# Optimization experiments

Hardware: AMD Instinct MI355X
Metric: run time of the kernel (lower is better)

## Reference

```python
import jax, jax.numpy as jnp
import numpy as np

T, H, I, E, K = 4096, 2048, 768, 64, 8  # tokens, hidden, moe_intermediate, experts, top_k


def setup_inputs() -> dict:
    key = jax.random.key(0)
    k1, k2, k3, k4 = jax.random.split(key, 4)
    return {
        "x": jax.random.normal(k1, (T, H), jnp.float32),
        "gate_w": jax.random.normal(k2, (E, H), jnp.float32) * 0.02,          # router weight [E, H]
        "w_gate_up": jax.random.normal(k3, (E, H, 2 * I), jnp.float32) * 0.02,  # stacked gate|up [E, H, 2I]
        "w_down": jax.random.normal(k4, (E, I, H), jnp.float32) * 0.02,        # stacked down [E, I, H]
        "top_k": K,
    }


def reference(x, gate_w, w_gate_up, w_down, top_k):
    n_tok, hidden = x.shape
    n_exp = gate_w.shape[0]
    inter = w_down.shape[1]

    # Router: softmax over experts (fp32 for stability), top-k, renormalize (norm_topk_prob)
    logits = x @ gate_w.T                                   # [T, E]
    probs = jax.nn.softmax(logits.astype(jnp.float32), axis=-1)
    top_p, top_i = jax.lax.top_k(probs, top_k)              # [T, K]
    top_p = top_p / jnp.sum(top_p, axis=-1, keepdims=True)

    # Scatter top-k weights into dense combine matrix [T, E] (top_k indices are distinct)
    combine = jnp.zeros((n_tok, n_exp), jnp.float32)
    combine = combine.at[jnp.arange(n_tok)[:, None], top_i].set(top_p)
    combine = combine.astype(x.dtype)

    # Per-expert SwiGLU MLP, accumulated via scan over the (fixed) expert axis.
    def body(acc, ws):
        wgu, wd, cw = ws                                    # [H,2I], [I,H], [T]
        gu = x @ wgu                                        # [T, 2I]
        h = jax.nn.silu(gu[:, :inter]) * gu[:, inter:]      # [T, I]
        return acc + (h @ wd) * cw[:, None], None

    out, _ = jax.lax.scan(body, jnp.zeros_like(x), (w_gate_up, w_down, combine.T))
    return out
```

## Files before the change

kernel.cpp:

```cpp
#include <hip/hip_runtime.h>
#include <hip/hip_bf16.h>
#include <cstdint>
#include <cstddef>

#define T_TOK 4096
#define HID   2048
#define INTER 768
#define NEXP  64

typedef float  f32x4  __attribute__((ext_vector_type(4)));
typedef __bf16 bf16x8 __attribute__((ext_vector_type(8)));
typedef __bf16 bf16x4 __attribute__((ext_vector_type(4)));

__device__ __forceinline__ void gl16(const void* g, void* l) {
  __builtin_amdgcn_global_load_lds((const __attribute__((address_space(1))) void*)g,
                                   (__attribute__((address_space(3))) void*)l, 16, 0, 0);
}

#define BAR() do { asm volatile("" ::: "memory"); __builtin_amdgcn_s_barrier(); asm volatile("" ::: "memory"); } while (0)


__global__ void zero_meta_kernel(int* counts, int* fill) {
  int t = threadIdx.x;
  if (t < NEXP) { counts[t] = 0; fill[t] = 0; }
}

__global__ void scan_kernel(const int* __restrict__ counts, int* __restrict__ offsets,
                            int* __restrict__ tb) {
  if (threadIdx.x == 0) {
    int s = 0, ts = 0;
    for (int e = 0; e < NEXP; e++) {
      offsets[e] = s; tb[e] = ts;
      s += counts[e]; ts += (counts[e] + 255) >> 8;
    }
    offsets[NEXP] = s; tb[NEXP] = ts;
  }
}

__global__ void scatter_kernel(const int* __restrict__ topk_id, const float* __restrict__ topk_w,
                               const int* __restrict__ offsets, int* __restrict__ fill,
                               int* __restrict__ pair_tok, float* __restrict__ pair_w,
                               int* __restrict__ pair_pos) {
  int i = blockIdx.x * 256 + threadIdx.x;
  int e = topk_id[i];
  int pos = offsets[e] + atomicAdd(&fill[e], 1);
  pair_tok[pos] = i >> 3;
  pair_w[pos]  = topk_w[i];
  pair_pos[i]  = pos;
}


__device__ __forceinline__ void transpose_tile(
    const float* __restrict__ src, __bf16* __restrict__ dst,
    int Kd, int Nd, int mode, int wid, char* Sw, int lane) {
  const int g = lane >> 4, nq = lane & 15;
  const int NT = Nd >> 6, KT = Kd >> 6, NB = Nd >> 7;
  int tpe = KT * NT;
  int e = wid / tpe;
  int rem = wid - e * tpe;
  int kt = rem / NT;
  int nt = rem - kt * NT;
  const float* sp = src + ((size_t)e * Kd + (size_t)kt * 64) * Nd + nt * 64;

  float4 vv[16];
  #pragma unroll
  for (int kq = 0; kq < 16; kq++)
    vv[kq] = *(const float4*)(sp + (size_t)(kq * 4 + g) * Nd + nq * 4);

  const int n_l = nq * 4 + g;
  #pragma unroll
  for (int kq = 0; kq < 16; kq++) {
    float4 v = vv[kq];
    float t0 = __shfl_xor(v.x, 32), t1 = __shfl_xor(v.y, 32);
    float t2 = __shfl_xor(v.z, 32), t3 = __shfl_xor(v.w, 32);
    bool hi2 = (g & 2) != 0;
    float a0 = hi2 ? t2 : v.x, a1 = hi2 ? t3 : v.y;
    float a2 = hi2 ? v.z : t0, a3 = hi2 ? v.w : t1;
    float s0 = __shfl_xor(a0, 16), s1 = __shfl_xor(a1, 16);
    float s2 = __shfl_xor(a2, 16), s3 = __shfl_xor(a3, 16);
    bool odd = (g & 1) != 0;
    float u0 = odd ? s1 : a0, u1 = odd ? a1 : s0;
    float u2 = odd ? s3 : a2, u3 = odd ? a3 : s2;
    bf16x4 b; b[0] = (__bf16)u0; b[1] = (__bf16)u1; b[2] = (__bf16)u2; b[3] = (__bf16)u3;
    *(bf16x4*)(Sw + n_l * 128 + ((kq ^ (n_l & 15)) << 3)) = b;
  }
  asm volatile("s_waitcnt lgkmcnt(0)" ::: "memory");
  __builtin_amdgcn_sched_barrier(0);

  if (mode == 0) {
    uint4* gdst = (uint4*)dst + ((((size_t)e * NB + (nt >> 1)) * KT + kt) << 10) + ((nt & 1) << 6) + lane;
    #pragma unroll
    for (int q = 0; q < 8; q++) {
      int p0 = (2 * q) ^ (lane & 15), p1 = (2 * q + 1) ^ (lane & 15);
      uint2 lo = *(const uint2*)(Sw + lane * 128 + (p0 << 3));
      uint2 hi = *(const uint2*)(Sw + lane * 128 + (p1 << 3));
      gdst[q * 128] = make_uint4(lo.x, lo.y, hi.x, hi.y);
    }
  } else {
    int n = nt * 64 + lane;
    int isup = (n >= INTER) ? 1 : 0;
    int hcol = isup ? n - INTER : n;
    int nb = hcol >> 7, ho = hcol & 127;
    int rp = isup * 128 + ho;
    uint4* gdst = (uint4*)dst + ((((size_t)e * 6 + nb) * KT + kt) << 11) + rp;
    #pragma unroll
    for (int q = 0; q < 8; q++) {
      int p0 = (2 * q) ^ (lane & 15), p1 = (2 * q + 1) ^ (lane & 15);
      uint2 lo = *(const uint2*)(Sw + lane * 128 + (p0 << 3));
      uint2 hi = *(const uint2*)(Sw + lane * 128 + (p1 << 3));
      gdst[q * 256] = make_uint4(lo.x, lo.y, hi.x, hi.y);
    }
  }
}


__global__ __launch_bounds__(256) void fat1_kernel(
    const float* __restrict__ x, const float* __restrict__ gw, __bf16* __restrict__ xbf,
    int* __restrict__ topk_id, float* __restrict__ topk_w, int* __restrict__ counts,
    const float* __restrict__ wgu, __bf16* __restrict__ w2gu) {
  __shared__ __align__(16) char fsm[32768];
  const int tid = threadIdx.x, lane = tid & 63, wv = tid >> 6;

  if (blockIdx.x >= 256) {
    transpose_tile(wgu, w2gu, HID, 2 * INTER, 1,
                   ((int)blockIdx.x - 256) * 4 + wv, fsm + wv * 8192, lane);
    return;
  }

  float (*gs)[65] = (float (*)[65])fsm;
  float (*xs)[65] = (float (*)[65])(fsm + 16640);
  const int tblk = blockIdx.x * 16;

  float acc[4] = {0.f, 0.f, 0.f, 0.f};
  for (int kc = 0; kc < HID; kc += 64) {
    #pragma unroll
    for (int i = 0; i < 4; i++) {
      int r = tid >> 2;
      int c = (tid & 3) * 16 + i * 4;
      float4 v = *(const float4*)(gw + (size_t)r * HID + kc + c);
      gs[r][c + 0] = v.x; gs[r][c + 1] = v.y; gs[r][c + 2] = v.z; gs[r][c + 3] = v.w;
    }
    {
      int r = tid >> 4;
      int c = (tid & 15) * 4;
      float4 v = *(const float4*)(x + (size_t)(tblk + r) * HID + kc + c);
      xs[r][c + 0] = v.x; xs[r][c + 1] = v.y; xs[r][c + 2] = v.z; xs[r][c + 3] = v.w;
      bf16x4 b;
      b[0] = (__bf16)v.x; b[1] = (__bf16)v.y; b[2] = (__bf16)v.z; b[3] = (__bf16)v.w;
      *(bf16x4*)(xbf + (size_t)(tblk + r) * HID + kc + c) = b;
    }
    __syncthreads();
    #pragma unroll 8
    for (int k = 0; k < 64; k++) {
      float g = gs[lane][k];
      #pragma unroll
      for (int j = 0; j < 4; j++) acc[j] = fmaf(xs[wv * 4 + j][k], g, acc[j]);
    }
    __syncthreads();
  }

  for (int j = 0; j < 4; j++) {
    int t = tblk + wv * 4 + j;
    float vsel = acc[j];
    float m1 = 0.f, denom = 0.f;
    int myid = 0; float myw = 0.f;
    for (int s = 0; s < 8; s++) {
      float bv = vsel; int bi = lane;
      #pragma unroll
      for (int off = 32; off > 0; off >>= 1) {
        float ov = __shfl_xor(bv, off);
        int   oi = __shfl_xor(bi, off);
        if (ov > bv || (ov == bv && oi < bi)) { bv = ov; bi = oi; }
      }
      if (s == 0) m1 = bv;
      float ev = __expf(bv - m1);
      denom += ev;
      if (lane == s)  { myid = bi; myw = ev; }
      if (lane == bi) vsel = -3.402823466e38f;
    }
    if (lane < 8) {
      topk_id[t * 8 + lane] = myid;
      topk_w[t * 8 + lane]  = myw / denom;
      atomicAdd(&counts[myid], 1);
    }
  }
}


__global__ __launch_bounds__(512, 2) void fat2_kernel(
    const uint4* __restrict__ xbf4, const uint4* __restrict__ w2gu,
    const int* __restrict__ offsets, const int* __restrict__ tb,
    const int* __restrict__ pair_tok, const float* __restrict__ pair_w,
    uint4* __restrict__ H2,
    const float* __restrict__ wd, __bf16* __restrict__ w2d, int nwgG1) {
  __shared__ __align__(16) char smem[131072];
  const int tid = threadIdx.x, lane = tid & 63, w = tid >> 6;
  const int bid = blockIdx.x;

  if (bid >= nwgG1) {
    transpose_tile(wd, w2d, INTER, HID, 0,
                   (bid - nwgG1) * 8 + w, smem + w * 8192, lane);
    return;
  }

  const int q8 = nwgG1 >> 3, r8 = nwgG1 & 7;
  const int xcd = bid & 7, idx = bid >> 3;
  const int wg = (xcd < r8 ? xcd * (q8 + 1) : r8 * (q8 + 1) + (xcd - r8) * q8) + idx;
  const int mt0 = wg % 3, t1 = wg / 3, nb = t1 % 6, e = t1 / 6;
  const int off = offsets[e], cnt = offsets[e + 1] - off;
  const uint4* Bb = w2gu + (size_t)(e * 6 + nb) * 65536;
  const int wm = w >> 2, wn = w & 3;
  const int g = lane >> 4, nq = lane & 15;

#define STA1(p, ks) do {                                                         \
    char* d_ = smem + (p) * 65536 + (w << 12);                                   \
    gl16(a0b + (size_t)(ks) * 8, d_ + (lane << 4));                              \
    gl16(a1b + (size_t)(ks) * 8, d_ + ((128 + lane) << 4)); } while (0)
#define STA2(p, ks) do {                                                         \
    char* d_ = smem + (p) * 65536 + (w << 12);                                   \
    gl16(a2b + (size_t)(ks) * 8, d_ + ((64 + lane) << 4));                       \
    gl16(a3b + (size_t)(ks) * 8, d_ + ((192 + lane) << 4)); } while (0)
#define STBG(p, ks) do { size_t so_ = (size_t)(ks) * 2048 + (w << 8);            \
    char* d_ = smem + (p) * 65536 + 32768 + (w << 12);                           \
    gl16(Bb + so_ + lane,       d_ + (lane << 4));                               \
    gl16(Bb + so_ + 64 + lane,  d_ + ((64 + lane) << 4)); } while (0)
#define STBU(p, ks) do { size_t so_ = (size_t)(ks) * 2048 + (w << 8);            \
    char* d_ = smem + (p) * 65536 + 32768 + (w << 12);                           \
    gl16(Bb + so_ + 128 + lane, d_ + ((128 + lane) << 4));                       \
    gl16(Bb + so_ + 192 + lane, d_ + ((192 + lane) << 4)); } while (0)

  for (int mt = mt0; mt * 256 < cnt; mt += 3) {
    const int rows = min(256, cnt - mt * 256);
    const int m0 = mt * 256;
    const int rm = rows - 1;
    const uint4* a0b = xbf4 + (size_t)pair_tok[off + m0 + min(lane, rm)]       * 256 + w;
    const uint4* a1b = xbf4 + (size_t)pair_tok[off + m0 + min(128 + lane, rm)] * 256 + w;
    const uint4* a2b = xbf4 + (size_t)pair_tok[off + m0 + min(64 + lane, rm)]  * 256 + w;
    const uint4* a3b = xbf4 + (size_t)pair_tok[off + m0 + min(192 + lane, rm)] * 256 + w;

    f32x4 ag[8][2], au[8][2];
    #pragma unroll
    for (int i = 0; i < 8; i++)
      #pragma unroll
      for (int j = 0; j < 2; j++)
        #pragma unroll
        for (int q = 0; q < 4; q++) { ag[i][j][q] = 0.f; au[i][j][q] = 0.f; }

    STA1(0, 0); STBG(0, 0); STBU(0, 0); STA2(0, 0);
    for (int ks = 0; ks < 32; ks++) {
      const int p = ks & 1;
      char* bA = smem + p * 65536;
      char* bB = bA + 32768;
      const bool pre = (ks + 1 < 32);
      bf16x8 af[4][2], bg[2][2], bu[2][2];
      asm volatile("s_waitcnt vmcnt(4)" ::: "memory");
      BAR();
      if (pre) STA1(p ^ 1, ks + 1);
      #pragma unroll
      for (int kk = 0; kk < 2; kk++) {
        const int q = kk * 4 + g;
        #pragma unroll
        for (int mi = 0; mi < 4; mi++)
          af[mi][kk] = *(const bf16x8*)(bA + (q << 12) + ((wm * 128 + mi * 16 + nq) << 4));
        #pragma unroll
        for (int ni = 0; ni < 2; ni++)
          bg[ni][kk] = *(const bf16x8*)(bB + (q << 12) + ((wn * 32 + ni * 16 + nq) << 4));
      }
      __builtin_amdgcn_s_setprio(1);
      #pragma unroll
      for (int kk = 0; kk < 2; kk++)
        #pragma unroll
        for (int mi = 0; mi < 4; mi++)
          #pragma unroll
          for (int ni = 0; ni < 2; ni++)
            ag[mi][ni] = __builtin_amdgcn_mfma_f32_16x16x32_bf16(af[mi][kk], bg[ni][kk], ag[mi][ni], 0, 0, 0);
      __builtin_amdgcn_s_setprio(0);
      if (pre) asm volatile("s_waitcnt vmcnt(4)" ::: "memory");
      else     asm volatile("s_waitcnt vmcnt(2)" ::: "memory");
      BAR();
      if (pre) STBG(p ^ 1, ks + 1);
      #pragma unroll
      for (int kk = 0; kk < 2; kk++) {
        const int q = kk * 4 + g;
        #pragma unroll
        for (int ni = 0; ni < 2; ni++)
          bu[ni][kk] = *(const bf16x8*)(bB + (q << 12) + ((128 + wn * 32 + ni * 16 + nq) << 4));
      }
      __builtin_amdgcn_s_setprio(1);
      #pragma unroll
      for (int kk = 0; kk < 2; kk++)
        #pragma unroll
        for (int mi = 0; mi < 4; mi++)
          #pragma unroll
          for (int ni = 0; ni < 2; ni++)
            au[mi][ni] = __builtin_amdgcn_mfma_f32_16x16x32_bf16(af[mi][kk], bu[ni][kk], au[mi][ni], 0, 0, 0);
      __builtin_amdgcn_s_setprio(0);
      if (pre) asm volatile("s_waitcnt vmcnt(4)" ::: "memory");
      else     asm volatile("s_waitcnt vmcnt(0)" ::: "memory");
      BAR();
      if (pre) STBU(p ^ 1, ks + 1);
      #pragma unroll
      for (int kk = 0; kk < 2; kk++) {
        const int q = kk * 4 + g;
        #pragma unroll
        for (int mi = 0; mi < 4; mi++)
          af[mi][kk] = *(const bf16x8*)(bA + (q << 12) + ((wm * 128 + 64 + mi * 16 + nq) << 4));
      }
      __builtin_amdgcn_s_setprio(1);
      #pragma unroll
      for (int kk = 0; kk < 2; kk++)
        #pragma unroll
        for (int mi = 0; mi < 4; mi++)
          #pragma unroll
          for (int ni = 0; ni < 2; ni++)
            ag[4 + mi][ni] = __builtin_amdgcn_mfma_f32_16x16x32_bf16(af[mi][kk], bg[ni][kk], ag[4 + mi][ni], 0, 0, 0);
      __builtin_amdgcn_s_setprio(0);
      BAR();
      if (pre) STA2(p ^ 1, ks + 1);
      __builtin_amdgcn_s_setprio(1);
      #pragma unroll
      for (int kk = 0; kk < 2; kk++)
        #pragma unroll
        for (int mi = 0; mi < 4; mi++)
          #pragma unroll
          for (int ni = 0; ni < 2; ni++)
            au[4 + mi][ni] = __builtin_amdgcn_mfma_f32_16x16x32_bf16(af[mi][kk], bu[ni][kk], au[4 + mi][ni], 0, 0, 0);
      __builtin_amdgcn_s_setprio(0);
    }

    #pragma unroll
    for (int mi = 0; mi < 8; mi++) {
      const int mrow = (mi < 4) ? (wm * 128 + mi * 16) : (wm * 128 + 64 + (mi - 4) * 16);
      #pragma unroll
      for (int reg = 0; reg < 4; reg++) {
        int rrow = mrow + g * 4 + reg;
        float pw = (rrow < rows) ? pair_w[off + m0 + rrow] : 0.f;
        #pragma unroll
        for (int ni = 0; ni < 2; ni++) {
          float gv = ag[mi][ni][reg];
          float uv = au[mi][ni][reg];
          float sv = gv / (1.f + __expf(-gv));
          int col = wn * 32 + ni * 16 + nq;
          *(__bf16*)(smem + rrow * 256 + ((col * 2) ^ ((rrow & 7) << 4))) = (__bf16)(sv * uv * pw);
        }
      }
    }
    BAR();
    {
      uint4* Hb = H2 + (size_t)(tb[e] + mt) * 24576 + nb * 16 * 256;
      #pragma unroll
      for (int i = 0; i < 8; i++) {
        int idx2 = tid + i * 512;
        int gx = idx2 >> 8, row = idx2 & 255;
        uint4 v = *(const uint4*)(smem + row * 256 + ((gx * 16) ^ ((row & 7) << 4)));
        Hb[gx * 256 + row] = v;
      }
    }
    BAR();
  }
#undef STA1
#undef STA2
#undef STBG
#undef STBU
}


__global__ __launch_bounds__(512, 2) void gemm2_kernel(
    const uint4* __restrict__ H2, const uint4* __restrict__ w2d,
    const int* __restrict__ offsets, const int* __restrict__ tb,
    __bf16* __restrict__ ybuf, int e0, int nwg) {
  __shared__ __align__(16) char smem[131072];
  const int bid = blockIdx.x;
  const int q8 = nwg >> 3, r8 = nwg & 7;
  const int xcd = bid & 7, idx = bid >> 3;
  const int wg = (xcd < r8 ? xcd * (q8 + 1) : r8 * (q8 + 1) + (xcd - r8) * q8) + idx;
  const int mt0 = wg % 3, t1 = wg / 3, nb2 = t1 % 8, ez = t1 / 8;
  const int e = e0 + ez;
  const int off = offsets[e], cnt = offsets[e + 1] - off;
  const uint4* Bw = w2d;
  const int pnl0 = ez * 16 + nb2 * 2, pnl1 = pnl0 + 1;
  const int tid = threadIdx.x, lane = tid & 63, w = tid >> 6;
  const int wm = w >> 2, wn = w & 3;
  const int g = lane >> 4, nq = lane & 15;

#define S2A1(p, ks) do { size_t so_ = (size_t)(ks) * 2048 + (w << 8);            \
    char* d_ = smem + (p) * 65536 + (w << 12);                                   \
    gl16(Ab + so_ + lane,       d_ + (lane << 4));                               \
    gl16(Ab + so_ + 128 + lane, d_ + ((128 + lane) << 4)); } while (0)
#define S2A2(p, ks) do { size_t so_ = (size_t)(ks) * 2048 + (w << 8);            \
    char* d_ = smem + (p) * 65536 + (w << 12);                                   \
    gl16(Ab + so_ + 64 + lane,  d_ + ((64 + lane) << 4));                        \
    gl16(Ab + so_ + 192 + lane, d_ + ((192 + lane) << 4)); } while (0)
#define S2BG(p, ks) do { size_t so_ = ((size_t)pnl0 * 12 + (ks)) * 1024 + (w << 7); \
    char* d_ = smem + (p) * 65536 + 32768 + (w << 12);                           \
    gl16(Bw + so_ + lane,      d_ + (lane << 4));                                \
    gl16(Bw + so_ + 64 + lane, d_ + ((64 + lane) << 4)); } while (0)
#define S2BH(p, ks) do { size_t so_ = ((size_t)pnl1 * 12 + (ks)) * 1024 + (w << 7); \
    char* d_ = smem + (p) * 65536 + 32768 + (w << 12);                           \
    gl16(Bw + so_ + lane,      d_ + ((128 + lane) << 4));                        \
    gl16(Bw + so_ + 64 + lane, d_ + ((192 + lane) << 4)); } while (0)

  for (int mt = mt0; mt * 256 < cnt; mt += 3) {
    const int rows = min(256, cnt - mt * 256);
    const uint4* Ab = H2 + (size_t)(tb[e] + mt) * 24576;

    f32x4 a0[8][2], a1[8][2];
    #pragma unroll
    for (int i = 0; i < 8; i++)
      #pragma unroll
      for (int j = 0; j < 2; j++)
        #pragma unroll
        for (int q = 0; q < 4; q++) { a0[i][j][q] = 0.f; a1[i][j][q] = 0.f; }

    S2A1(0, 0); S2BG(0, 0); S2BH(0, 0); S2A2(0, 0);
    for (int ks = 0; ks < 12; ks++) {
      const int p = ks & 1;
      char* bA = smem + p * 65536;
      char* bB = bA + 32768;
      const bool pre = (ks + 1 < 12);
      bf16x8 af[4][2], bl[2][2], bh[2][2];
      asm volatile("s_waitcnt vmcnt(4)" ::: "memory");
      BAR();
      if (pre) S2A1(p ^ 1, ks + 1);
      #pragma unroll
      for (int kk = 0; kk < 2; kk++) {
        const int q = kk * 4 + g;
        #pragma unroll
        for (int mi = 0; mi < 4; mi++)
          af[mi][kk] = *(const bf16x8*)(bA + (q << 12) + ((wm * 128 + mi * 16 + nq) << 4));
        #pragma unroll
        for (int ni = 0; ni < 2; ni++)
          bl[ni][kk] = *(const bf16x8*)(bB + (q << 12) + ((wn * 32 + ni * 16 + nq) << 4));
      }
      __builtin_amdgcn_s_setprio(1);
      #pragma unroll
      for (int kk = 0; kk < 2; kk++)
        #pragma unroll
        for (int mi = 0; mi < 4; mi++)
          #pragma unroll
          for (int ni = 0; ni < 2; ni++)
            a0[mi][ni] = __builtin_amdgcn_mfma_f32_16x16x32_bf16(af[mi][kk], bl[ni][kk], a0[mi][ni], 0, 0, 0);
      __builtin_amdgcn_s_setprio(0);
      if (pre) asm volatile("s_waitcnt vmcnt(4)" ::: "memory");
      else     asm volatile("s_waitcnt vmcnt(2)" ::: "memory");
      BAR();
      if (pre) S2BG(p ^ 1, ks + 1);
      #pragma unroll
      for (int kk = 0; kk < 2; kk++) {
        const int q = kk * 4 + g;
        #pragma unroll
        for (int ni = 0; ni < 2; ni++)
          bh[ni][kk] = *(const bf16x8*)(bB + (q << 12) + ((128 + wn * 32 + ni * 16 + nq) << 4));
      }
      __builtin_amdgcn_s_setprio(1);
      #pragma unroll
      for (int kk = 0; kk < 2; kk++)
        #pragma unroll
        for (int mi = 0; mi < 4; mi++)
          #pragma unroll
          for (int ni = 0; ni < 2; ni++)
            a1[mi][ni] = __builtin_amdgcn_mfma_f32_16x16x32_bf16(af[mi][kk], bh[ni][kk], a1[mi][ni], 0, 0, 0);
      __builtin_amdgcn_s_setprio(0);
      if (pre) asm volatile("s_waitcnt vmcnt(4)" ::: "memory");
      else     asm volatile("s_waitcnt vmcnt(0)" ::: "memory");
      BAR();
      if (pre) S2BH(p ^ 1, ks + 1);
      #pragma unroll
      for (int kk = 0; kk < 2; kk++) {
        const int q = kk * 4 + g;
        #pragma unroll
        for (int mi = 0; mi < 4; mi++)
          af[mi][kk] = *(const bf16x8*)(bA + (q << 12) + ((wm * 128 + 64 + mi * 16 + nq) << 4));
      }
      __builtin_amdgcn_s_setprio(1);
      #pragma unroll
      for (int kk = 0; kk < 2; kk++)
        #pragma unroll
        for (int mi = 0; mi < 4; mi++)
          #pragma unroll
          for (int ni = 0; ni < 2; ni++)
            a0[4 + mi][ni] = __builtin_amdgcn_mfma_f32_16x16x32_bf16(af[mi][kk], bl[ni][kk], a0[4 + mi][ni], 0, 0, 0);
      __builtin_amdgcn_s_setprio(0);
      BAR();
      if (pre) S2A2(p ^ 1, ks + 1);
      __builtin_amdgcn_s_setprio(1);
      #pragma unroll
      for (int kk = 0; kk < 2; kk++)
        #pragma unroll
        for (int mi = 0; mi < 4; mi++)
          #pragma unroll
          for (int ni = 0; ni < 2; ni++)
            a1[4 + mi][ni] = __builtin_amdgcn_mfma_f32_16x16x32_bf16(af[mi][kk], bh[ni][kk], a1[4 + mi][ni], 0, 0, 0);
      __builtin_amdgcn_s_setprio(0);
    }

    const int m0 = mt * 256;
    #pragma unroll
    for (int mi = 0; mi < 8; mi++) {
      const int mrow = (mi < 4) ? (wm * 128 + mi * 16) : (wm * 128 + 64 + (mi - 4) * 16);
      #pragma unroll
      for (int reg = 0; reg < 4; reg++) {
        int rrow = mrow + g * 4 + reg;
        if (rrow < rows) {
          __bf16* yrow = ybuf + (size_t)(off + m0 + rrow) * HID + nb2 * 256 + wn * 32;
          #pragma unroll
          for (int ni = 0; ni < 2; ni++) {
            yrow[ni * 16 + nq]       = (__bf16)a0[mi][ni][reg];
            yrow[128 + ni * 16 + nq] = (__bf16)a1[mi][ni][reg];
          }
        }
      }
    }
  }
#undef S2A1
#undef S2A2
#undef S2BG
#undef S2BH
}


__global__ __launch_bounds__(256) void reduce_kernel(
    const __bf16* __restrict__ ybuf, const int* __restrict__ pair_pos,
    float* __restrict__ out) {
  const int t = blockIdx.x, j = threadIdx.x;
  const int* pp = pair_pos + t * 8;
  float s[8] = {0.f, 0.f, 0.f, 0.f, 0.f, 0.f, 0.f, 0.f};
  #pragma unroll
  for (int k = 0; k < 8; k++) {
    bf16x8 v = *(const bf16x8*)(ybuf + (size_t)pp[k] * HID + j * 8);
    #pragma unroll
    for (int c = 0; c < 8; c++) s[c] += (float)v[c];
  }
  float4 o0 = make_float4(s[0], s[1], s[2], s[3]);
  float4 o1 = make_float4(s[4], s[5], s[6], s[7]);
  *(float4*)(out + (size_t)t * HID + j * 8) = o0;
  *(float4*)(out + (size_t)t * HID + j * 8 + 4) = o1;
}


extern "C" void kernel_launch(void* const* d_in, const int* in_sizes, int n_in,
                              void* d_out, int out_size, void* d_ws, size_t ws_size,
                              hipStream_t stream) {
  const float* x   = (const float*)d_in[0];
  const float* gw  = (const float*)d_in[1];
  const float* wgu = (const float*)d_in[2];
  const float* wd  = (const float*)d_in[3];
  float* out = (float*)d_out;

  char* ws = (char*)d_ws;
  int*   counts   = (int*)(ws + 0);
  int*   fill     = (int*)(ws + 256);
  int*   offsets  = (int*)(ws + 512);
  int*   tb       = (int*)(ws + 1024);
  int*   topk_id  = (int*)(ws + 4096);
  float* topk_w   = (float*)(ws + 135168);
  int*   pair_tok = (int*)(ws + 266240);
  float* pair_w   = (float*)(ws + 397312);
  int*   pair_pos = (int*)(ws + 528384);
  __bf16* xbf  = (__bf16*)(ws + 1048576);
  __bf16* ybuf = (__bf16*)(ws + 68157440);
  uint4*  H2   = (uint4*)(ws + 537919488);
  const size_t w2_base = 613416960ull;
  __bf16* w2gu = (__bf16*)(ws + w2_base);
  __bf16* w2d  = (__bf16*)(ws + w2_base + 64ull * 6291456ull);

  zero_meta_kernel<<<1, 128, 0, stream>>>(counts, fill);
  fat1_kernel<<<256 + 12288, 256, 0, stream>>>(x, gw, xbf, topk_id, topk_w, counts, wgu, w2gu);
  scan_kernel<<<1, 64, 0, stream>>>(counts, offsets, tb);
  scatter_kernel<<<128, 256, 0, stream>>>(topk_id, topk_w, offsets, fill, pair_tok, pair_w, pair_pos);

  fat2_kernel<<<1152 + 3072, 512, 0, stream>>>((const uint4*)xbf, (const uint4*)w2gu,
                                               offsets, tb, pair_tok, pair_w, H2,
                                               wd, w2d, 1152);
  gemm2_kernel<<<1536, 512, 0, stream>>>(H2, (const uint4*)w2d, offsets, tb, ybuf, 0, 1536);
  reduce_kernel<<<T_TOK, 256, 0, stream>>>(ybuf, pair_pos, out);
}
```

Before: 966.1 us.

## Triple-buffer A tiles in LDS to prefetch gathered tokens two steps ahead

The gate/up GEMM now keeps three LDS stages for the gathered activation (A) tiles and two for the weight (B) tiles, raising shared memory from 128 KB to 160 KB. A loads are issued two k-steps ahead while B loads stay one step ahead, and the vmcnt waits are retuned to match the deeper pipeline. The aim is to hide the latency of the scattered token-row gathers. The cost is more LDS per block, which may reduce how many blocks fit per CU under the 2-block launch bound, plus more complex wait accounting.

```diff
diff --git a/kernel.cpp b/kernel.cpp
--- a/kernel.cpp
+++ b/kernel.cpp
@@ -193,7 +193,7 @@
     const int* __restrict__ pair_tok, const float* __restrict__ pair_w,
     uint4* __restrict__ H2,
     const float* __restrict__ wd, __bf16* __restrict__ w2d, int nwgG1) {
-  __shared__ __align__(16) char smem[131072];
+  __shared__ __align__(16) char smem[163840];
   const int tid = threadIdx.x, lane = tid & 63, w = tid >> 6;
   const int bid = blockIdx.x;
 
@@ -212,20 +212,20 @@
   const int wm = w >> 2, wn = w & 3;
   const int g = lane >> 4, nq = lane & 15;
 
-#define STA1(p, ks) do {                                                         \
-    char* d_ = smem + (p) * 65536 + (w << 12);                                   \
+#define STA1(s, ks) do {                                                         \
+    char* d_ = smem + (s) * 32768 + (w << 12);                                   \
     gl16(a0b + (size_t)(ks) * 8, d_ + (lane << 4));                              \
     gl16(a1b + (size_t)(ks) * 8, d_ + ((128 + lane) << 4)); } while (0)
-#define STA2(p, ks) do {                                                         \
-    char* d_ = smem + (p) * 65536 + (w << 12);                                   \
+#define STA2(s, ks) do {                                                         \
+    char* d_ = smem + (s) * 32768 + (w << 12);                                   \
     gl16(a2b + (size_t)(ks) * 8, d_ + ((64 + lane) << 4));                       \
     gl16(a3b + (size_t)(ks) * 8, d_ + ((192 + lane) << 4)); } while (0)
-#define STBG(p, ks) do { size_t so_ = (size_t)(ks) * 2048 + (w << 8);            \
-    char* d_ = smem + (p) * 65536 + 32768 + (w << 12);                           \
+#define STBG(pb, ks) do { size_t so_ = (size_t)(ks) * 2048 + (w << 8);           \
+    char* d_ = smem + 98304 + (pb) * 32768 + (w << 12);                          \
     gl16(Bb + so_ + lane,       d_ + (lane << 4));                               \
     gl16(Bb + so_ + 64 + lane,  d_ + ((64 + lane) << 4)); } while (0)
-#define STBU(p, ks) do { size_t so_ = (size_t)(ks) * 2048 + (w << 8);            \
-    char* d_ = smem + (p) * 65536 + 32768 + (w << 12);                           \
+#define STBU(pb, ks) do { size_t so_ = (size_t)(ks) * 2048 + (w << 8);           \
+    char* d_ = smem + 98304 + (pb) * 32768 + (w << 12);                          \
     gl16(Bb + so_ + 128 + lane, d_ + ((128 + lane) << 4));                       \
     gl16(Bb + so_ + 192 + lane, d_ + ((192 + lane) << 4)); } while (0)
 
@@ -246,16 +246,16 @@
         #pragma unroll
         for (int q = 0; q < 4; q++) { ag[i][j][q] = 0.f; au[i][j][q] = 0.f; }
 
-    STA1(0, 0); STBG(0, 0); STBU(0, 0); STA2(0, 0);
+    STA1(0, 0); STA2(0, 0); STBG(0, 0); STBU(0, 0); STA1(1, 1); STA2(1, 1);
     for (int ks = 0; ks < 32; ks++) {
-      const int p = ks & 1;
-      char* bA = smem + p * 65536;
-      char* bB = bA + 32768;
-      const bool pre = (ks + 1 < 32);
+      char* bA = smem + (ks % 3) * 32768;
+      const int pb = ks & 1;
+      char* bB = smem + 98304 + pb * 32768;
       bf16x8 af[4][2], bg[2][2], bu[2][2];
-      asm volatile("s_waitcnt vmcnt(4)" ::: "memory");
-      BAR();
-      if (pre) STA1(p ^ 1, ks + 1);
+      if (ks < 31) asm volatile("s_waitcnt vmcnt(6)" ::: "memory");
+      else         asm volatile("s_waitcnt vmcnt(2)" ::: "memory");
+      BAR();
+      if (ks + 1 < 32) STBG(pb ^ 1, ks + 1);
       #pragma unroll
       for (int kk = 0; kk < 2; kk++) {
         const int q = kk * 4 + g;
@@ -275,10 +275,10 @@
           for (int ni = 0; ni < 2; ni++)
             ag[mi][ni] = __builtin_amdgcn_mfma_f32_16x16x32_bf16(af[mi][kk], bg[ni][kk], ag[mi][ni], 0, 0, 0);
       __builtin_amdgcn_s_setprio(0);
-      if (pre) asm volatile("s_waitcnt vmcnt(4)" ::: "memory");
-      else     asm volatile("s_waitcnt vmcnt(2)" ::: "memory");
-      BAR();
-      if (pre) STBG(p ^ 1, ks + 1);
+      if (ks < 31) asm volatile("s_waitcnt vmcnt(6)" ::: "memory");
+      else         asm volatile("s_waitcnt vmcnt(0)" ::: "memory");
+      BAR();
+      if (ks + 1 < 32) STBU(pb ^ 1, ks + 1);
       #pragma unroll
       for (int kk = 0; kk < 2; kk++) {
         const int q = kk * 4 + g;
@@ -295,10 +295,8 @@
           for (int ni = 0; ni < 2; ni++)
             au[mi][ni] = __builtin_amdgcn_mfma_f32_16x16x32_bf16(af[mi][kk], bu[ni][kk], au[mi][ni], 0, 0, 0);
       __builtin_amdgcn_s_setprio(0);
-      if (pre) asm volatile("s_waitcnt vmcnt(4)" ::: "memory");
-      else     asm volatile("s_waitcnt vmcnt(0)" ::: "memory");
-      BAR();
-      if (pre) STBU(p ^ 1, ks + 1);
+      BAR();
+      if (ks + 2 < 32) STA1((ks + 2) % 3, ks + 2);
       #pragma unroll
       for (int kk = 0; kk < 2; kk++) {
         const int q = kk * 4 + g;
@@ -316,7 +314,7 @@
             ag[4 + mi][ni] = __builtin_amdgcn_mfma_f32_16x16x32_bf16(af[mi][kk], bg[ni][kk], ag[4 + mi][ni], 0, 0, 0);
       __builtin_amdgcn_s_setprio(0);
       BAR();
-      if (pre) STA2(p ^ 1, ks + 1);
+      if (ks + 2 < 32) STA2((ks + 2) % 3, ks + 2);
       __builtin_amdgcn_s_setprio(1);
       #pragma unroll
       for (int kk = 0; kk < 2; kk++)
```

New measurement: 949.2 us. Within noise of the previous version (-1.8%).
